# Performance work log

Measured on AMD Instinct MI355X. Metric: run time of the kernel, lower is better.

Reference implementation:

```python
import jax, jax.numpy as jnp
import numpy as np

H = 128  # hidden size
IN = 18  # input features


def _lstm_layer(x, Wih, Whh, bih, bhh):
    # x: [B, T, D_in]; Wih: [4H, D_in]; Whh: [4H, H]
    B = x.shape[0]
    h0 = jnp.zeros((B, H), x.dtype)
    c0 = jnp.zeros((B, H), x.dtype)
    # Precompute input projections for all timesteps (one big GEMM).
    x_proj = jnp.einsum('btd,gd->btg', x, Wih) + bih + bhh  # [B, T, 4H]
    xs = jnp.swapaxes(x_proj, 0, 1)  # [T, B, 4H]

    def step(carry, xt):
        h, c = carry
        gates = xt + h @ Whh.T  # [B, 4H]
        i, f, g, o = jnp.split(gates, 4, axis=-1)  # PyTorch gate order: i,f,g,o
        i = jax.nn.sigmoid(i)
        f = jax.nn.sigmoid(f)
        g = jnp.tanh(g)
        o = jax.nn.sigmoid(o)
        c = f * c + i * g
        h = o * jnp.tanh(c)
        return (h, c), h

    (_, _), hs = jax.lax.scan(step, (h0, c0), xs)
    return jnp.swapaxes(hs, 0, 1)  # [B, T, H]


def setup_inputs() -> dict:
    key = jax.random.key(0)
    ks = jax.random.split(key, 16)
    B, T = 512, 512
    s_h = 1.0 / np.sqrt(H)
    u = lambda k, shape, s: jax.random.uniform(k, shape, jnp.float32, -s, s)
    return {
        'x': jax.random.normal(ks[0], (B, T, IN), jnp.float32),
        'W_ih0': u(ks[1], (4 * H, IN), s_h), 'W_hh0': u(ks[2], (4 * H, H), s_h),
        'b_ih0': u(ks[3], (4 * H,), s_h), 'b_hh0': u(ks[4], (4 * H,), s_h),
        'W_ih1': u(ks[5], (4 * H, H), s_h), 'W_hh1': u(ks[6], (4 * H, H), s_h),
        'b_ih1': u(ks[7], (4 * H,), s_h), 'b_hh1': u(ks[8], (4 * H,), s_h),
        'W_fc1': u(ks[9], (64, H), 1.0 / np.sqrt(H)), 'b_fc1': u(ks[10], (64,), 1.0 / np.sqrt(H)),
        'W_fc2': u(ks[11], (1, 64), 1.0 / np.sqrt(64)), 'b_fc2': u(ks[12], (1,), 1.0 / np.sqrt(64)),
    }


def reference(x, W_ih0, W_hh0, b_ih0, b_hh0, W_ih1, W_hh1, b_ih1, b_hh1,
              W_fc1, b_fc1, W_fc2, b_fc2):
    # Eval mode: inter-layer and head dropout are identity.
    h1 = _lstm_layer(x, W_ih0, W_hh0, b_ih0, b_hh0)   # [B, T, H]
    h2 = _lstm_layer(h1, W_ih1, W_hh1, b_ih1, b_hh1)  # [B, T, H]
    last = h2[:, -1, :]                                # [B, H]
    out = jax.nn.relu(last @ W_fc1.T + b_fc1)          # [B, 64]
    out = out @ W_fc2.T + b_fc2                        # [B, 1]
    return jax.nn.sigmoid(out)
```

## Files before the change

kernel.cpp:

```cpp
#include <hip/hip_runtime.h>
#include <stdint.h>

typedef short bf8 __attribute__((ext_vector_type(8)));
typedef float f4  __attribute__((ext_vector_type(4)));
typedef unsigned short u16;
typedef unsigned long long u64;

#define LOG2E 1.4426950408889634f

__device__ __forceinline__ u16 f2bf(float f){
  uint32_t u = __builtin_bit_cast(uint32_t, f);
  u += 0x7fffu + ((u >> 16) & 1u);
  return (u16)(u >> 16);
}

__device__ __forceinline__ float lstm_cell(float ai, float af, float ag, float ao, float& c){
  float Ei = __builtin_amdgcn_exp2f(-ai);
  float Ef = __builtin_amdgcn_exp2f(-af);
  float Eg = __builtin_amdgcn_exp2f(-ag);
  float Eo = __builtin_amdgcn_exp2f(-ao);
  float m1  = (1.f + Ei) * (1.f + Eg);
  float a3  = 1.f + Ef;
  float num = fmaf(c, m1, (1.f - Eg) * a3);
  c = num * __builtin_amdgcn_rcpf(a3 * m1);
  float Ec = __builtin_amdgcn_exp2f(c * (-2.f * LOG2E));
  return (1.f - Ec) * __builtin_amdgcn_rcpf((1.f + Eo) * (1.f + Ec));
}

__global__ void prep_kernel(const float* __restrict__ Wih0, const float* __restrict__ Whh0,
                            const float* __restrict__ bih0, const float* __restrict__ bhh0,
                            const float* __restrict__ Wih1, const float* __restrict__ Whh1,
                            const float* __restrict__ bih1, const float* __restrict__ bhh1,
                            u16* __restrict__ W0c, u16* __restrict__ W1c,
                            float* __restrict__ bias0, float* __restrict__ bias1,
                            int* __restrict__ prog){
  int g = blockIdx.x;
  int t = threadIdx.x;
  float s = (g >= 256 && g < 384) ? 2.0f * LOG2E : LOG2E;
  for(int k = t; k < 160; k += 64){
    float v = 0.0f;
    if(k < 128)      v = Whh0[g*128 + k];
    else if(k < 146) v = Wih0[g*18 + (k-128)];
    W0c[g*160 + k] = f2bf(v * s);
  }
  for(int k = t; k < 256; k += 64){
    float v = (k < 128) ? Whh1[g*128 + k] : Wih1[g*128 + (k-128)];
    W1c[g*256 + k] = f2bf(v * s);
  }
  if(t == 0){
    bias0[g] = (bih0[g] + bhh0[g]) * s;
    bias1[g] = (bih1[g] + bhh1[g]) * s;
  }
  if(g == 0 && t < 32) prog[t] = 0;
}

__global__ __launch_bounds__(512, 1)
void lstm_fused(const u16* __restrict__ Wc0, const u16* __restrict__ Wc1,
                const float* __restrict__ bias0, const float* __restrict__ bias1,
                const float* __restrict__ xin,
                u64* __restrict__ h1g,
                int* __restrict__ prog,
                const float* __restrict__ Wfc1, const float* __restrict__ bfc1,
                const float* __restrict__ Wfc2, const float* __restrict__ bfc2,
                float* __restrict__ out)
{
  __shared__ __align__(16) u16  hb[2][16][136];
  __shared__ __align__(16) u16  xb[2][16][40];
  __shared__ __align__(16) u16  h2b[2][16][136];
  __shared__ __align__(16) u16  ring[4][16][136];
  __shared__ __align__(16) float ffin[16][132];

  const int tid  = threadIdx.x;
  const int wave = tid >> 6;
  const int lane = tid & 63;
  const int quad = lane >> 4;
  const int l15  = lane & 15;
  const bool isL0 = (blockIdx.x < 32);
  const int rb   = isL0 ? blockIdx.x : (blockIdx.x - 32);
  const int rowbase = rb * 16;

  if(isL0){
    bf8 Ah[4][4], Ax[4];
#pragma unroll
    for(int q = 0; q < 4; q++){
      const u16* wp = Wc0 + (u64)(128*q + 16*wave + l15)*160 + quad*8;
#pragma unroll
      for(int kt = 0; kt < 4; kt++) Ah[q][kt] = *(const bf8*)(wp + kt*32);
      Ax[q] = *(const bf8*)(wp + 128);
    }
    f4 bini[4];
#pragma unroll
    for(int q = 0; q < 4; q++) bini[q] = *(const f4*)(bias0 + 128*q + 16*wave + quad*4);
    float c[4] = {0.f,0.f,0.f,0.f};

    for(int i = tid; i < 2*16*136; i += 512) ((u16*)hb)[i] = 0;
    for(int i = tid; i < 2*16*40;  i += 512) ((u16*)xb)[i] = 0;
    __syncthreads();

    int sr = 0, sk = 0;
    if(tid < 288){
      sr = tid/18; sk = tid - 18*sr;
      xb[0][sr][sk] = f2bf(xin[((u64)(rowbase+sr)*512 + 0)*18 + sk]);
      xb[1][sr][sk] = f2bf(xin[((u64)(rowbase+sr)*512 + 1)*18 + sk]);
    }
    float xv = 0.f;
    if(tid < 288) xv = xin[((u64)(rowbase+sr)*512 + 2)*18 + sk];
    __syncthreads();

    f4 pre[4];
    {
      bf8 Bx = *(const bf8*)(&xb[0][l15][quad*8]);
#pragma unroll
      for(int q = 0; q < 4; q++)
        pre[q] = __builtin_amdgcn_mfma_f32_16x16x32_bf16(Ax[q], Bx, bini[q], 0,0,0);
    }
    __syncthreads();

    for(int t = 0; t < 512; t++){
      const int cur = t & 1, nxt = cur ^ 1;
      if(tid < 288){
        if(t <= 509) xb[t & 1][sr][sk] = f2bf(xv);
        const int tl = (t + 3 < 512) ? t + 3 : 511;
        xv = xin[((u64)(rowbase+sr)*512 + tl)*18 + sk];
      }

      bf8 B[4];
      const u16* br = &hb[cur][l15][quad*8];
#pragma unroll
      for(int kt = 0; kt < 4; kt++) B[kt] = *(const bf8*)(br + kt*32);

      f4 acc[4];
#pragma unroll
      for(int q = 0; q < 4; q++){
        f4 a = pre[q];
#pragma unroll
        for(int kt = 0; kt < 4; kt++)
          a = __builtin_amdgcn_mfma_f32_16x16x32_bf16(Ah[q][kt], B[kt], a, 0,0,0);
        acc[q] = a;
      }

      u64 hpack; u16* hp = (u16*)&hpack;
#pragma unroll
      for(int r = 0; r < 4; r++)
        hp[r] = f2bf(lstm_cell(acc[0][r], acc[1][r], acc[2][r], acc[3][r], c[r]));

      *(u64*)(&hb[nxt][l15][16*wave + quad*4]) = hpack;
      __hip_atomic_store(h1g + ((u64)t*512 + rowbase + l15)*32 + 4*wave + quad,
                         hpack, __ATOMIC_RELAXED, __HIP_MEMORY_SCOPE_AGENT);

      if(t < 511){
        bf8 Bx = *(const bf8*)(&xb[(t+1) & 1][l15][quad*8]);
#pragma unroll
        for(int q = 0; q < 4; q++)
          pre[q] = __builtin_amdgcn_mfma_f32_16x16x32_bf16(Ax[q], Bx, bini[q], 0,0,0);
      }

      __builtin_amdgcn_sched_barrier(0);
      if(wave < 5) asm volatile("s_waitcnt vmcnt(4) lgkmcnt(0)" ::: "memory");
      else         asm volatile("s_waitcnt vmcnt(2) lgkmcnt(0)" ::: "memory");
      __builtin_amdgcn_s_barrier();
      __builtin_amdgcn_sched_barrier(0);
      if(tid == 0 && t > 0)
        __hip_atomic_store(prog + rb, t - 1, __ATOMIC_RELAXED, __HIP_MEMORY_SCOPE_AGENT);
    }
    asm volatile("s_waitcnt vmcnt(0)" ::: "memory");
    __builtin_amdgcn_s_barrier();
    if(tid == 0)
      __hip_atomic_store(prog + rb, 512, __ATOMIC_RELAXED, __HIP_MEMORY_SCOPE_AGENT);
  } else {
    bf8 A2[4][4], A1[4][4];
#pragma unroll
    for(int q = 0; q < 4; q++){
      const u16* wp = Wc1 + (u64)(128*q + 16*wave + l15)*256 + quad*8;
#pragma unroll
      for(int kt = 0; kt < 4; kt++){
        A2[q][kt] = *(const bf8*)(wp + kt*32);
        A1[q][kt] = *(const bf8*)(wp + 128 + kt*32);
      }
    }
    f4 bini[4];
#pragma unroll
    for(int q = 0; q < 4; q++) bini[q] = *(const f4*)(bias1 + 128*q + 16*wave + quad*4);
    float c[4] = {0.f,0.f,0.f,0.f};

    for(int i = tid; i < 2*16*136; i += 512) ((u16*)h2b)[i] = 0;

    const int pr = tid >> 5;
    const int pu = tid & 31;
    int seen = 0;
    __syncthreads();

    while(seen < 2){
      seen = __hip_atomic_load(prog + rb, __ATOMIC_ACQUIRE, __HIP_MEMORY_SCOPE_AGENT);
      if(seen < 2) __builtin_amdgcn_s_sleep(2);
    }
    {
      u64 v0 = __hip_atomic_load(h1g + ((u64)0*512 + rowbase + pr)*32 + pu,
                                 __ATOMIC_RELAXED, __HIP_MEMORY_SCOPE_AGENT);
      *(u64*)(&ring[0][pr][pu*4]) = v0;
      u64 v1 = __hip_atomic_load(h1g + ((u64)1*512 + rowbase + pr)*32 + pu,
                                 __ATOMIC_RELAXED, __HIP_MEMORY_SCOPE_AGENT);
      *(u64*)(&ring[1][pr][pu*4]) = v1;
    }
    while(seen < 3){
      seen = __hip_atomic_load(prog + rb, __ATOMIC_ACQUIRE, __HIP_MEMORY_SCOPE_AGENT);
      if(seen < 3) __builtin_amdgcn_s_sleep(2);
    }
    u64 pv = __hip_atomic_load(h1g + ((u64)2*512 + rowbase + pr)*32 + pu,
                               __ATOMIC_RELAXED, __HIP_MEMORY_SCOPE_AGENT);
    __syncthreads();

    f4 pre[4];
    {
      const u16* rr = &ring[0][l15][quad*8];
#pragma unroll
      for(int q = 0; q < 4; q++){
        f4 a = bini[q];
#pragma unroll
        for(int kt = 0; kt < 4; kt++)
          a = __builtin_amdgcn_mfma_f32_16x16x32_bf16(A1[q][kt], *(const bf8*)(rr + kt*32), a, 0,0,0);
        pre[q] = a;
      }
    }

    float hv[4] = {0.f,0.f,0.f,0.f};
    for(int t = 0; t < 512; t++){
      const int cur = t & 1, nxt = cur ^ 1;

      bf8 B2[4];
      const u16* br2 = &h2b[cur][l15][quad*8];
#pragma unroll
      for(int kt = 0; kt < 4; kt++) B2[kt] = *(const bf8*)(br2 + kt*32);

      u64 pnew = 0;
      if(t <= 508){
        const int need = t + 4;
        while(seen < need){
          seen = __hip_atomic_load(prog + rb, __ATOMIC_ACQUIRE, __HIP_MEMORY_SCOPE_AGENT);
          if(seen < need) __builtin_amdgcn_s_sleep(2);
        }
        pnew = __hip_atomic_load(h1g + ((u64)(t+3)*512 + rowbase + pr)*32 + pu,
                                 __ATOMIC_RELAXED, __HIP_MEMORY_SCOPE_AGENT);
      }

      f4 acc[4];
#pragma unroll
      for(int q = 0; q < 4; q++){
        f4 a = pre[q];
#pragma unroll
        for(int kt = 0; kt < 4; kt++)
          a = __builtin_amdgcn_mfma_f32_16x16x32_bf16(A2[q][kt], B2[kt], a, 0,0,0);
        acc[q] = a;
      }

      if(t < 511){
        const u16* rr = &ring[(t+1) & 3][l15][quad*8];
#pragma unroll
        for(int q = 0; q < 4; q++){
          f4 a = bini[q];
#pragma unroll
          for(int kt = 0; kt < 4; kt++)
            a = __builtin_amdgcn_mfma_f32_16x16x32_bf16(A1[q][kt], *(const bf8*)(rr + kt*32), a, 0,0,0);
          pre[q] = a;
        }
      }

      if(t <= 509) *(u64*)(&ring[(t+2) & 3][pr][pu*4]) = pv;

      u64 hpack; u16* hp = (u16*)&hpack;
#pragma unroll
      for(int r = 0; r < 4; r++){
        hv[r] = lstm_cell(acc[0][r], acc[1][r], acc[2][r], acc[3][r], c[r]);
        hp[r] = f2bf(hv[r]);
      }
      *(u64*)(&h2b[nxt][l15][16*wave + quad*4]) = hpack;

      __builtin_amdgcn_sched_barrier(0);
      asm volatile("s_waitcnt lgkmcnt(0)" ::: "memory");
      __builtin_amdgcn_s_barrier();
      __builtin_amdgcn_sched_barrier(0);

      pv = pnew;
    }
#pragma unroll
    for(int r = 0; r < 4; r++) ffin[l15][16*wave + quad*4 + r] = hv[r];
    __syncthreads();

    {
      int r = tid >> 5, u = tid & 31;
      float s0 = bfc1[2*u], s1 = bfc1[2*u+1];
      const float* w0 = Wfc1 + (2*u)*128;
      const float* w1 = Wfc1 + (2*u+1)*128;
      for(int j = 0; j < 128; j++){
        float h = ffin[r][j];
        s0 = fmaf(w0[j], h, s0);
        s1 = fmaf(w1[j], h, s1);
      }
      float term = fmaxf(s0, 0.f)*Wfc2[2*u] + fmaxf(s1, 0.f)*Wfc2[2*u+1];
#pragma unroll
      for(int off = 16; off > 0; off >>= 1) term += __shfl_down(term, off, 32);
      if(u == 0){
        float z = (term + bfc2[0]) * LOG2E;
        out[rowbase + r] = __builtin_amdgcn_rcpf(1.0f + __builtin_amdgcn_exp2f(-z));
      }
    }
  }
}

extern "C" void kernel_launch(void* const* d_in, const int* in_sizes, int n_in,
                              void* d_out, int out_size, void* d_ws, size_t ws_size,
                              hipStream_t stream){
  const float* x    = (const float*)d_in[0];
  const float* Wih0 = (const float*)d_in[1];
  const float* Whh0 = (const float*)d_in[2];
  const float* bih0 = (const float*)d_in[3];
  const float* bhh0 = (const float*)d_in[4];
  const float* Wih1 = (const float*)d_in[5];
  const float* Whh1 = (const float*)d_in[6];
  const float* bih1 = (const float*)d_in[7];
  const float* bhh1 = (const float*)d_in[8];
  const float* Wfc1 = (const float*)d_in[9];
  const float* bfc1 = (const float*)d_in[10];
  const float* Wfc2 = (const float*)d_in[11];
  const float* bfc2 = (const float*)d_in[12];

  char* ws = (char*)d_ws;
  u16*   W0c   = (u16*)(ws);
  u16*   W1c   = (u16*)(ws + 163840);
  float* bias0 = (float*)(ws + 163840 + 262144);
  float* bias1 = bias0 + 512;
  int*   prog  = (int*)(ws + 163840 + 262144 + 4096);
  u64*   h1g   = (u64*)(ws + 163840 + 262144 + 4096 + 256);

  prep_kernel<<<dim3(512), dim3(64), 0, stream>>>(Wih0, Whh0, bih0, bhh0,
                                                  Wih1, Whh1, bih1, bhh1,
                                                  W0c, W1c, bias0, bias1, prog);

  lstm_fused<<<dim3(64), dim3(512), 0, stream>>>(
      W0c, W1c, bias0, bias1, x, h1g, prog,
      Wfc1, bfc1, Wfc2, bfc2, (float*)d_out);
}
```

Baseline: 635.9 us.

## Deepen layer-1 h1 prefetch ring and hoist LDS operand loads ahead of MFMAs

The layer-1 blocks' h1 staging ring grows from 4 to 8 slots, and the prefetch distance grows from 3 to 5 timesteps. This loosens the coupling to layer-0 progress so consumers spin less on the progress flag. The next-step input-projection operands are now loaded from LDS at the top of the step and the projection MFMAs are moved before the cell math in both layers, so load latency overlaps the recurrent MFMAs. The x-staging lanes are respread across all waves so the per-wave vmcnt wait can be uniform. The cost is more LDS, more registers and a longer startup wait for layer 1.

```diff
diff --git a/kernel.cpp b/kernel.cpp
--- a/kernel.cpp
+++ b/kernel.cpp
@@ -67,7 +67,7 @@
   __shared__ __align__(16) u16  hb[2][16][136];
   __shared__ __align__(16) u16  xb[2][16][40];
   __shared__ __align__(16) u16  h2b[2][16][136];
-  __shared__ __align__(16) u16  ring[4][16][136];
+  __shared__ __align__(16) u16  ring[8][16][136];
   __shared__ __align__(16) float ffin[16][132];
 
   const int tid  = threadIdx.x;
@@ -97,14 +97,15 @@
     for(int i = tid; i < 2*16*40;  i += 512) ((u16*)xb)[i] = 0;
     __syncthreads();
 
-    int sr = 0, sk = 0;
-    if(tid < 288){
-      sr = tid/18; sk = tid - 18*sr;
+    const bool xl = (lane < 36);
+    const int  sr = 2*wave + (lane >= 18 ? 1 : 0);
+    const int  sk = lane - (lane >= 18 ? 18 : 0);
+    if(xl){
       xb[0][sr][sk] = f2bf(xin[((u64)(rowbase+sr)*512 + 0)*18 + sk]);
       xb[1][sr][sk] = f2bf(xin[((u64)(rowbase+sr)*512 + 1)*18 + sk]);
     }
     float xv = 0.f;
-    if(tid < 288) xv = xin[((u64)(rowbase+sr)*512 + 2)*18 + sk];
+    if(xl) xv = xin[((u64)(rowbase+sr)*512 + 2)*18 + sk];
     __syncthreads();
 
     f4 pre[4];
@@ -118,7 +119,7 @@
 
     for(int t = 0; t < 512; t++){
       const int cur = t & 1, nxt = cur ^ 1;
-      if(tid < 288){
+      if(xl){
         if(t <= 509) xb[t & 1][sr][sk] = f2bf(xv);
         const int tl = (t + 3 < 512) ? t + 3 : 511;
         xv = xin[((u64)(rowbase+sr)*512 + tl)*18 + sk];
@@ -128,6 +129,7 @@
       const u16* br = &hb[cur][l15][quad*8];
 #pragma unroll
       for(int kt = 0; kt < 4; kt++) B[kt] = *(const bf8*)(br + kt*32);
+      bf8 Bxn = *(const bf8*)(&xb[(t+1) & 1][l15][quad*8]);
 
       f4 acc[4];
 #pragma unroll
@@ -139,6 +141,12 @@
         acc[q] = a;
       }
 
+      if(t < 511){
+#pragma unroll
+        for(int q = 0; q < 4; q++)
+          pre[q] = __builtin_amdgcn_mfma_f32_16x16x32_bf16(Ax[q], Bxn, bini[q], 0,0,0);
+      }
+
       u64 hpack; u16* hp = (u16*)&hpack;
 #pragma unroll
       for(int r = 0; r < 4; r++)
@@ -148,16 +156,8 @@
       __hip_atomic_store(h1g + ((u64)t*512 + rowbase + l15)*32 + 4*wave + quad,
                          hpack, __ATOMIC_RELAXED, __HIP_MEMORY_SCOPE_AGENT);
 
-      if(t < 511){
-        bf8 Bx = *(const bf8*)(&xb[(t+1) & 1][l15][quad*8]);
-#pragma unroll
-        for(int q = 0; q < 4; q++)
-          pre[q] = __builtin_amdgcn_mfma_f32_16x16x32_bf16(Ax[q], Bx, bini[q], 0,0,0);
-      }
-
       __builtin_amdgcn_sched_barrier(0);
-      if(wave < 5) asm volatile("s_waitcnt vmcnt(4) lgkmcnt(0)" ::: "memory");
-      else         asm volatile("s_waitcnt vmcnt(2) lgkmcnt(0)" ::: "memory");
+      asm volatile("s_waitcnt vmcnt(4) lgkmcnt(0)" ::: "memory");
       __builtin_amdgcn_s_barrier();
       __builtin_amdgcn_sched_barrier(0);
       if(tid == 0 && t > 0)
@@ -190,23 +190,17 @@
     int seen = 0;
     __syncthreads();
 
-    while(seen < 2){
+    while(seen < 5){
       seen = __hip_atomic_load(prog + rb, __ATOMIC_ACQUIRE, __HIP_MEMORY_SCOPE_AGENT);
-      if(seen < 2) __builtin_amdgcn_s_sleep(2);
-    }
-    {
-      u64 v0 = __hip_atomic_load(h1g + ((u64)0*512 + rowbase + pr)*32 + pu,
-                                 __ATOMIC_RELAXED, __HIP_MEMORY_SCOPE_AGENT);
-      *(u64*)(&ring[0][pr][pu*4]) = v0;
-      u64 v1 = __hip_atomic_load(h1g + ((u64)1*512 + rowbase + pr)*32 + pu,
-                                 __ATOMIC_RELAXED, __HIP_MEMORY_SCOPE_AGENT);
-      *(u64*)(&ring[1][pr][pu*4]) = v1;
-    }
-    while(seen < 3){
-      seen = __hip_atomic_load(prog + rb, __ATOMIC_ACQUIRE, __HIP_MEMORY_SCOPE_AGENT);
-      if(seen < 3) __builtin_amdgcn_s_sleep(2);
-    }
-    u64 pv = __hip_atomic_load(h1g + ((u64)2*512 + rowbase + pr)*32 + pu,
+      if(seen < 5) __builtin_amdgcn_s_sleep(2);
+    }
+#pragma unroll
+    for(int s = 0; s < 4; s++){
+      u64 v = __hip_atomic_load(h1g + ((u64)s*512 + rowbase + pr)*32 + pu,
+                                __ATOMIC_RELAXED, __HIP_MEMORY_SCOPE_AGENT);
+      *(u64*)(&ring[s][pr][pu*4]) = v;
+    }
+    u64 pv = __hip_atomic_load(h1g + ((u64)4*512 + rowbase + pr)*32 + pu,
                                __ATOMIC_RELAXED, __HIP_MEMORY_SCOPE_AGENT);
     __syncthreads();
 
@@ -227,19 +221,22 @@
     for(int t = 0; t < 512; t++){
       const int cur = t & 1, nxt = cur ^ 1;
 
-      bf8 B2[4];
+      bf8 B2[4], B1n[4];
       const u16* br2 = &h2b[cur][l15][quad*8];
 #pragma unroll
       for(int kt = 0; kt < 4; kt++) B2[kt] = *(const bf8*)(br2 + kt*32);
+      const u16* br1 = &ring[(t+1) & 7][l15][quad*8];
+#pragma unroll
+      for(int kt = 0; kt < 4; kt++) B1n[kt] = *(const bf8*)(br1 + kt*32);
 
       u64 pnew = 0;
-      if(t <= 508){
-        const int need = t + 4;
+      if(t <= 506){
+        const int need = t + 6;
         while(seen < need){
           seen = __hip_atomic_load(prog + rb, __ATOMIC_ACQUIRE, __HIP_MEMORY_SCOPE_AGENT);
           if(seen < need) __builtin_amdgcn_s_sleep(2);
         }
-        pnew = __hip_atomic_load(h1g + ((u64)(t+3)*512 + rowbase + pr)*32 + pu,
+        pnew = __hip_atomic_load(h1g + ((u64)(t+5)*512 + rowbase + pr)*32 + pu,
                                  __ATOMIC_RELAXED, __HIP_MEMORY_SCOPE_AGENT);
       }
 
@@ -254,18 +251,17 @@
       }
 
       if(t < 511){
-        const u16* rr = &ring[(t+1) & 3][l15][quad*8];
 #pragma unroll
         for(int q = 0; q < 4; q++){
           f4 a = bini[q];
 #pragma unroll
           for(int kt = 0; kt < 4; kt++)
-            a = __builtin_amdgcn_mfma_f32_16x16x32_bf16(A1[q][kt], *(const bf8*)(rr + kt*32), a, 0,0,0);
+            a = __builtin_amdgcn_mfma_f32_16x16x32_bf16(A1[q][kt], B1n[kt], a, 0,0,0);
           pre[q] = a;
         }
       }
 
-      if(t <= 509) *(u64*)(&ring[(t+2) & 3][pr][pu*4]) = pv;
+      if(t <= 507) *(u64*)(&ring[(t+4) & 7][pr][pu*4]) = pv;
 
       u64 hpack; u16* hp = (u16*)&hpack;
 #pragma unroll
```

Result: slower. 662.4 us (+4.2%).

## Load layer-0 hidden states directly into MFMA operand registers, drop LDS ring

Applied to the files above, without the earlier changes.

The layer-1 blocks no longer stage layer-0 outputs through a shared-memory ring buffer. Each lane now loads its MFMA B-operand fragments straight from global memory into registers, double-buffered across a two-step unrolled loop, with a prefetch depth of two steps instead of three. This removes the LDS writes and reads for the ring, but each lane issues more small global loads, and the shorter lookahead may expose more of the cross-block latency.

```diff
diff --git a/kernel.cpp b/kernel.cpp
--- a/kernel.cpp
+++ b/kernel.cpp
@@ -5,6 +5,8 @@
 typedef float f4  __attribute__((ext_vector_type(4)));
 typedef unsigned short u16;
 typedef unsigned long long u64;
+
+struct u64x2 { u64 a, b; };
 
 #define LOG2E 1.4426950408889634f
 
@@ -67,7 +69,6 @@
   __shared__ __align__(16) u16  hb[2][16][136];
   __shared__ __align__(16) u16  xb[2][16][40];
   __shared__ __align__(16) u16  h2b[2][16][136];
-  __shared__ __align__(16) u16  ring[4][16][136];
   __shared__ __align__(16) float ffin[16][132];
 
   const int tid  = threadIdx.x;
@@ -149,10 +150,10 @@
                          hpack, __ATOMIC_RELAXED, __HIP_MEMORY_SCOPE_AGENT);
 
       if(t < 511){
-        bf8 Bx = *(const bf8*)(&xb[(t+1) & 1][l15][quad*8]);
+        bf8 Bxn = *(const bf8*)(&xb[(t+1) & 1][l15][quad*8]);
 #pragma unroll
         for(int q = 0; q < 4; q++)
-          pre[q] = __builtin_amdgcn_mfma_f32_16x16x32_bf16(Ax[q], Bx, bini[q], 0,0,0);
+          pre[q] = __builtin_amdgcn_mfma_f32_16x16x32_bf16(Ax[q], Bxn, bini[q], 0,0,0);
       }
 
       __builtin_amdgcn_sched_barrier(0);
@@ -185,8 +186,6 @@
 
     for(int i = tid; i < 2*16*136; i += 512) ((u16*)h2b)[i] = 0;
 
-    const int pr = tid >> 5;
-    const int pu = tid & 31;
     int seen = 0;
     __syncthreads();
 
@@ -194,94 +193,98 @@
       seen = __hip_atomic_load(prog + rb, __ATOMIC_ACQUIRE, __HIP_MEMORY_SCOPE_AGENT);
       if(seen < 2) __builtin_amdgcn_s_sleep(2);
     }
+    f4 pre[4];
+    bf8 Fa[4], Fb[4];
     {
-      u64 v0 = __hip_atomic_load(h1g + ((u64)0*512 + rowbase + pr)*32 + pu,
-                                 __ATOMIC_RELAXED, __HIP_MEMORY_SCOPE_AGENT);
-      *(u64*)(&ring[0][pr][pu*4]) = v0;
-      u64 v1 = __hip_atomic_load(h1g + ((u64)1*512 + rowbase + pr)*32 + pu,
-                                 __ATOMIC_RELAXED, __HIP_MEMORY_SCOPE_AGENT);
-      *(u64*)(&ring[1][pr][pu*4]) = v1;
-    }
-    while(seen < 3){
-      seen = __hip_atomic_load(prog + rb, __ATOMIC_ACQUIRE, __HIP_MEMORY_SCOPE_AGENT);
-      if(seen < 3) __builtin_amdgcn_s_sleep(2);
-    }
-    u64 pv = __hip_atomic_load(h1g + ((u64)2*512 + rowbase + pr)*32 + pu,
-                               __ATOMIC_RELAXED, __HIP_MEMORY_SCOPE_AGENT);
-    __syncthreads();
-
-    f4 pre[4];
-    {
-      const u16* rr = &ring[0][l15][quad*8];
+      const u64* gp0 = h1g + ((u64)0*512 + rowbase + l15)*32 + quad*2;
+      bf8 T0[4];
+#pragma unroll
+      for(int kt = 0; kt < 4; kt++){
+        u64 lo = __hip_atomic_load(gp0 + kt*8,     __ATOMIC_RELAXED, __HIP_MEMORY_SCOPE_AGENT);
+        u64 hi = __hip_atomic_load(gp0 + kt*8 + 1, __ATOMIC_RELAXED, __HIP_MEMORY_SCOPE_AGENT);
+        u64x2 u{lo, hi};
+        T0[kt] = __builtin_bit_cast(bf8, u);
+      }
 #pragma unroll
       for(int q = 0; q < 4; q++){
         f4 a = bini[q];
 #pragma unroll
         for(int kt = 0; kt < 4; kt++)
-          a = __builtin_amdgcn_mfma_f32_16x16x32_bf16(A1[q][kt], *(const bf8*)(rr + kt*32), a, 0,0,0);
+          a = __builtin_amdgcn_mfma_f32_16x16x32_bf16(A1[q][kt], T0[kt], a, 0,0,0);
         pre[q] = a;
       }
+      const u64* gp1 = h1g + ((u64)1*512 + rowbase + l15)*32 + quad*2;
+#pragma unroll
+      for(int kt = 0; kt < 4; kt++){
+        u64 lo = __hip_atomic_load(gp1 + kt*8,     __ATOMIC_RELAXED, __HIP_MEMORY_SCOPE_AGENT);
+        u64 hi = __hip_atomic_load(gp1 + kt*8 + 1, __ATOMIC_RELAXED, __HIP_MEMORY_SCOPE_AGENT);
+        u64x2 u{lo, hi};
+        Fa[kt] = __builtin_bit_cast(bf8, u);
+      }
     }
 
     float hv[4] = {0.f,0.f,0.f,0.f};
-    for(int t = 0; t < 512; t++){
-      const int cur = t & 1, nxt = cur ^ 1;
-
-      bf8 B2[4];
-      const u16* br2 = &h2b[cur][l15][quad*8];
-#pragma unroll
-      for(int kt = 0; kt < 4; kt++) B2[kt] = *(const bf8*)(br2 + kt*32);
-
-      u64 pnew = 0;
-      if(t <= 508){
-        const int need = t + 4;
-        while(seen < need){
-          seen = __hip_atomic_load(prog + rb, __ATOMIC_ACQUIRE, __HIP_MEMORY_SCOPE_AGENT);
-          if(seen < need) __builtin_amdgcn_s_sleep(2);
-        }
-        pnew = __hip_atomic_load(h1g + ((u64)(t+3)*512 + rowbase + pr)*32 + pu,
-                                 __ATOMIC_RELAXED, __HIP_MEMORY_SCOPE_AGENT);
-      }
-
-      f4 acc[4];
-#pragma unroll
-      for(int q = 0; q < 4; q++){
-        f4 a = pre[q];
-#pragma unroll
-        for(int kt = 0; kt < 4; kt++)
-          a = __builtin_amdgcn_mfma_f32_16x16x32_bf16(A2[q][kt], B2[kt], a, 0,0,0);
-        acc[q] = a;
-      }
-
-      if(t < 511){
-        const u16* rr = &ring[(t+1) & 3][l15][quad*8];
-#pragma unroll
-        for(int q = 0; q < 4; q++){
-          f4 a = bini[q];
-#pragma unroll
-          for(int kt = 0; kt < 4; kt++)
-            a = __builtin_amdgcn_mfma_f32_16x16x32_bf16(A1[q][kt], *(const bf8*)(rr + kt*32), a, 0,0,0);
-          pre[q] = a;
-        }
-      }
-
-      if(t <= 509) *(u64*)(&ring[(t+2) & 3][pr][pu*4]) = pv;
-
-      u64 hpack; u16* hp = (u16*)&hpack;
-#pragma unroll
-      for(int r = 0; r < 4; r++){
-        hv[r] = lstm_cell(acc[0][r], acc[1][r], acc[2][r], acc[3][r], c[r]);
-        hp[r] = f2bf(hv[r]);
-      }
-      *(u64*)(&h2b[nxt][l15][16*wave + quad*4]) = hpack;
-
-      __builtin_amdgcn_sched_barrier(0);
-      asm volatile("s_waitcnt lgkmcnt(0)" ::: "memory");
-      __builtin_amdgcn_s_barrier();
-      __builtin_amdgcn_sched_barrier(0);
-
-      pv = pnew;
-    }
+
+#define L1_STEP(T, BCUR, BNEXT)                                                          \
+    do{                                                                                  \
+      const int cur_ = (T) & 1, nxt_ = cur_ ^ 1;                                         \
+      if((T) <= 509){                                                                    \
+        const int need_ = (T) + 3;                                                       \
+        while(seen < need_){                                                             \
+          seen = __hip_atomic_load(prog + rb, __ATOMIC_ACQUIRE, __HIP_MEMORY_SCOPE_AGENT); \
+          if(seen < need_) __builtin_amdgcn_s_sleep(2);                                  \
+        }                                                                                \
+        const u64* gp_ = h1g + ((u64)((T)+2)*512 + rowbase + l15)*32 + quad*2;           \
+        _Pragma("unroll")                                                                \
+        for(int kt = 0; kt < 4; kt++){                                                   \
+          u64 lo_ = __hip_atomic_load(gp_ + kt*8,     __ATOMIC_RELAXED, __HIP_MEMORY_SCOPE_AGENT); \
+          u64 hi_ = __hip_atomic_load(gp_ + kt*8 + 1, __ATOMIC_RELAXED, __HIP_MEMORY_SCOPE_AGENT); \
+          u64x2 u_{lo_, hi_};                                                            \
+          BNEXT[kt] = __builtin_bit_cast(bf8, u_);                                       \
+        }                                                                                \
+      }                                                                                  \
+      bf8 B2_[4];                                                                        \
+      const u16* br2_ = &h2b[cur_][l15][quad*8];                                         \
+      _Pragma("unroll")                                                                  \
+      for(int kt = 0; kt < 4; kt++) B2_[kt] = *(const bf8*)(br2_ + kt*32);               \
+      f4 acc_[4];                                                                        \
+      _Pragma("unroll")                                                                  \
+      for(int q = 0; q < 4; q++){                                                        \
+        f4 a_ = pre[q];                                                                  \
+        _Pragma("unroll")                                                                \
+        for(int kt = 0; kt < 4; kt++)                                                    \
+          a_ = __builtin_amdgcn_mfma_f32_16x16x32_bf16(A2[q][kt], B2_[kt], a_, 0,0,0);   \
+        acc_[q] = a_;                                                                    \
+      }                                                                                  \
+      if((T) < 511){                                                                     \
+        _Pragma("unroll")                                                                \
+        for(int q = 0; q < 4; q++){                                                      \
+          f4 a_ = bini[q];                                                               \
+          _Pragma("unroll")                                                              \
+          for(int kt = 0; kt < 4; kt++)                                                  \
+            a_ = __builtin_amdgcn_mfma_f32_16x16x32_bf16(A1[q][kt], BCUR[kt], a_, 0,0,0);\
+          pre[q] = a_;                                                                   \
+        }                                                                                \
+      }                                                                                  \
+      u64 hpack_; u16* hp_ = (u16*)&hpack_;                                              \
+      _Pragma("unroll")                                                                  \
+      for(int r = 0; r < 4; r++){                                                        \
+        hv[r] = lstm_cell(acc_[0][r], acc_[1][r], acc_[2][r], acc_[3][r], c[r]);         \
+        hp_[r] = f2bf(hv[r]);                                                            \
+      }                                                                                  \
+      *(u64*)(&h2b[nxt_][l15][16*wave + quad*4]) = hpack_;                               \
+      __builtin_amdgcn_sched_barrier(0);                                                 \
+      asm volatile("s_waitcnt lgkmcnt(0)" ::: "memory");                                 \
+      __builtin_amdgcn_s_barrier();                                                      \
+      __builtin_amdgcn_sched_barrier(0);                                                 \
+    }while(0)
+
+    for(int tt = 0; tt < 512; tt += 2){
+      L1_STEP(tt,     Fa, Fb);
+      L1_STEP(tt + 1, Fb, Fa);
+    }
+#undef L1_STEP
+
 #pragma unroll
     for(int r = 0; r < 4; r++) ffin[l15][16*wave + quad*4 + r] = hv[r];
     __syncthreads();
```

New measurement: 1.111 ms. +74.8%, slower.
